# Kernel optimization log

Measured on AMD Instinct MI355X. Metric: run time of the kernel, lower is better.

The kernel has to match this reference:

```python
import jax, jax.numpy as jnp
import numpy as np

B, S, H, L = 32, 2048, 768, 9


def setup_inputs() -> dict:
    key = jax.random.key(0)
    k0, k1, k2, k3, k4, k5 = jax.random.split(key, 6)
    return {
        "hidden_states": jax.random.normal(k0, (B, S, H), jnp.float32),
        "W": jax.random.normal(k1, (L, H), jnp.float32) * 0.02,
        "b": jnp.zeros((L,), jnp.float32),
        "start_transitions": jax.random.uniform(k2, (L,), jnp.float32, -0.1, 0.1),
        "end_transitions": jax.random.uniform(k3, (L,), jnp.float32, -0.1, 0.1),
        "transitions": jax.random.uniform(k4, (L, L), jnp.float32, -0.1, 0.1),
        "labels": jax.random.randint(k5, (B, S), 0, L).astype(jnp.int64),
        "attention_mask": jnp.ones((B, S), jnp.int32),
    }


def _crf_neg_log_likelihood(emissions, tags, mask, start_transitions, end_transitions, transitions):
    # emissions: [B,S,L], tags: [B,S] int, mask: [B,S] bool (mask[:,0] assumed True)
    Bsz = emissions.shape[0]
    em_t = jnp.swapaxes(emissions, 0, 1)          # [S,B,L]
    tags_t = jnp.swapaxes(tags, 0, 1)             # [S,B]
    mask_t = jnp.swapaxes(mask, 0, 1).astype(emissions.dtype)  # [S,B]
    barange = jnp.arange(Bsz)

    # ---- numerator: score of the gold path (pytorch-crf _compute_score) ----
    score0 = start_transitions[tags_t[0]] + em_t[0][barange, tags_t[0]]  # [B]

    def num_step(score, x):
        em_i, tag_prev, tag_i, m_i = x
        step = transitions[tag_prev, tag_i] + em_i[barange, tag_i]
        return score + step * m_i, None

    score, _ = jax.lax.scan(num_step, score0,
                            (em_t[1:], tags_t[:-1], tags_t[1:], mask_t[1:]))
    seq_ends = jnp.sum(mask, axis=1).astype(jnp.int32) - 1              # [B]
    last_tags = jnp.take_along_axis(tags, seq_ends[:, None], axis=1)[:, 0]
    score = score + end_transitions[last_tags]

    # ---- denominator: log partition (forward algorithm) ----
    alpha0 = start_transitions[None, :] + em_t[0]  # [B,L]

    def den_step(alpha, x):
        em_i, m_i = x
        # alpha[b,i] + transitions[i,j] + em_i[b,j] -> logsumexp over i
        nxt = jax.nn.logsumexp(alpha[:, :, None] + transitions[None, :, :]
                               + em_i[:, None, :], axis=1)
        alpha = jnp.where(m_i[:, None] > 0, nxt, alpha)
        return alpha, None

    alpha, _ = jax.lax.scan(den_step, alpha0, (em_t[1:], mask_t[1:]))
    denom = jax.nn.logsumexp(alpha + end_transitions[None, :], axis=1)  # [B]

    llh = score - denom
    return -jnp.mean(llh)  # reduction='mean', loss = -log_likelihood


def reference(hidden_states, W, b, start_transitions, end_transitions, transitions, labels, attention_mask):
    # classifier over backbone hidden states
    emissions = jnp.einsum('bsh,lh->bsl', hidden_states, W) + b  # [B,S,L]
    label_mask = labels != -100
    lab = jnp.where(labels == -100, 0, labels)
    loss = _crf_neg_log_likelihood(emissions, lab, label_mask,
                                   start_transitions, end_transitions, transitions)
    return loss, emissions
```

## Files before the change

### kernel.cpp

```cpp
#include <hip/hip_runtime.h>

#define BB 32
#define SS 2048
#define HH 768
#define LL 9
#define NROWS (BB * SS)
#define NCHUNK 64
#define TCHUNK 32
#define PASSES 8
#define ROWS_PER_BLOCK 16
#define GEMM_BLOCKS (NROWS / ROWS_PER_BLOCK)

__device__ __forceinline__ float lse9(const float* v) {
  float m = fmaxf(fmaxf(fmaxf(fmaxf(v[0], v[1]), fmaxf(v[2], v[3])),
                        fmaxf(fmaxf(v[4], v[5]), fmaxf(v[6], v[7]))),
                  v[8]);
  float s = 0.f;
#pragma unroll
  for (int k = 0; k < 9; ++k) s += __expf(v[k] - m);
  return m + __logf(s);
}

template <int CTRL>
__device__ __forceinline__ float dpp_add(float x) {
  int t = __builtin_amdgcn_update_dpp(0, __float_as_int(x), CTRL, 0xf, 0xf, true);
  return x + __int_as_float(t);
}
__device__ __forceinline__ float red16(float x) {
  x = dpp_add<0xB1>(x);
  x = dpp_add<0x4E>(x);
  x = dpp_add<0x141>(x);
  x = dpp_add<0x140>(x);
  return x;
}

__global__ __launch_bounds__(256)
void emis_gemm(const float* __restrict__ hs, const float* __restrict__ W,
               const float* __restrict__ bias, float* __restrict__ em) {
  const int tid = threadIdx.x;
  const int lane = tid & 63;
  const int w = tid >> 6;
  const int pair = w >> 1;
  const int half = w & 1;
  const int rowbase = blockIdx.x * ROWS_PER_BLOCK;
  const int kb = half * 384;

  __shared__ float part[ROWS_PER_BLOCK][8][LL];

  float wr[LL][6];
#pragma unroll
  for (int l = 0; l < LL; ++l) {
    float4 t4 = *reinterpret_cast<const float4*>(W + l * HH + kb + lane * 4);
    float2 t2 = *reinterpret_cast<const float2*>(W + l * HH + kb + 256 + lane * 2);
    wr[l][0] = t4.x; wr[l][1] = t4.y; wr[l][2] = t4.z; wr[l][3] = t4.w;
    wr[l][4] = t2.x; wr[l][5] = t2.y;
  }

  const float* r0 = hs + (size_t)(rowbase + 0 * 2 + pair) * HH + kb;
  float4 a4 = *reinterpret_cast<const float4*>(r0 + lane * 4);
  float2 a2 = *reinterpret_cast<const float2*>(r0 + 256 + lane * 2);
  const float* r1 = hs + (size_t)(rowbase + 1 * 2 + pair) * HH + kb;
  float4 b4 = *reinterpret_cast<const float4*>(r1 + lane * 4);
  float2 b2 = *reinterpret_cast<const float2*>(r1 + 256 + lane * 2);

#pragma unroll
  for (int p = 0; p < PASSES; ++p) {
    float4 c4{};
    float2 c2{};
    if (p + 2 < PASSES) {
      const float* rn = hs + (size_t)(rowbase + (p + 2) * 2 + pair) * HH + kb;
      c4 = *reinterpret_cast<const float4*>(rn + lane * 4);
      c2 = *reinterpret_cast<const float2*>(rn + 256 + lane * 2);
    }
    const float h[6] = {a4.x, a4.y, a4.z, a4.w, a2.x, a2.y};
    if ((lane & 15) == 0) {
    }
    float acc[LL];
#pragma unroll
    for (int l = 0; l < LL; ++l) {
      float s = h[0] * wr[l][0];
#pragma unroll
      for (int q = 1; q < 6; ++q) s = fmaf(h[q], wr[l][q], s);
      acc[l] = red16(s);
    }
    if ((lane & 15) == 0) {
      const int pi = half * 4 + (lane >> 4);
      const int o = p * 2 + pair;
#pragma unroll
      for (int l = 0; l < LL; ++l) part[o][pi][l] = acc[l];
    }
    a4 = b4; a2 = b2; b4 = c4; b2 = c2;
  }
  __syncthreads();

  for (int j = tid; j < ROWS_PER_BLOCK * LL; j += 256) {
    const int o = j / LL, l = j - o * LL;
    float s = bias[l];
#pragma unroll
    for (int q = 0; q < 8; ++q) s += part[o][q][l];
    em[(size_t)(rowbase + o) * LL + l] = s;
  }
}

__global__ __launch_bounds__(128)
void crf_chunk(const float* __restrict__ em, const int* __restrict__ lab,
               const float* __restrict__ trans, const float* __restrict__ startT,
               float* __restrict__ Pout, float* __restrict__ numpart,
               int* __restrict__ cntpart) {
  const int blk = blockIdx.x;
  const int b = blk >> 6, c = blk & 63;
  const int tid = threadIdx.x;
  const int lane = tid & 63;
  const int wv = tid >> 6;
  __shared__ float em_s[TCHUNK * LL];
  __shared__ int lab_s[TCHUNK + 1];
  __shared__ float Pbuf[2][81];

  const int t0 = c * TCHUNK;
  const size_t ebase = (size_t)(b * SS + t0) * LL;
  for (int i = tid; i < TCHUNK * LL; i += 128) em_s[i] = em[ebase + i];
  if (tid <= TCHUNK) {
    int g = t0 - 1 + tid;
    lab_s[tid] = (g >= 0) ? lab[b * SS + g] : 0;
  }
  const int i9 = tid / 9, j9 = tid % 9;
  float tc[9];
  if (tid < 81) {
#pragma unroll
    for (int k = 0; k < 9; ++k) tc[k] = trans[k * 9 + j9];
  }
  __syncthreads();

  unsigned long long mb =
      __ballot((lane < 32) ? (lab_s[1 + lane] != -100) : false);
  unsigned mask32 = (unsigned)mb;

  if (wv == 1) {
    float sc = 0.f;
    if (lane < 32) {
      int lv = lab_s[1 + lane];
      int tg = (lv != -100) ? lv : 0;
      if (t0 + lane == 0) {
        sc = startT[tg] + em_s[tg];
      } else if (lv != -100) {
        int pv = lab_s[lane];
        int tp = (pv != -100) ? pv : 0;
        sc = trans[tp * LL + tg] + em_s[lane * LL + tg];
      }
    }
#pragma unroll
    for (int off = 32; off; off >>= 1) sc += __shfl_xor(sc, off, 64);
    if (lane == 0) {
      numpart[blk] = sc;
      cntpart[blk] = __popc(mask32);
    }
  }

  if (tid < 81) Pbuf[0][tid] = (i9 == j9) ? 0.f : -1e30f;
  __syncthreads();
  int cur = 0;
  const int ltstart = (c == 0) ? 1 : 0;
  for (int lt = ltstart; lt < TCHUNK; ++lt) {
    if ((mask32 >> lt) & 1u) {
      if (tid < 81) {
        float v[9];
#pragma unroll
        for (int k = 0; k < 9; ++k) v[k] = Pbuf[cur][i9 * 9 + k] + tc[k];
        Pbuf[cur ^ 1][tid] = lse9(v) + em_s[lt * LL + j9];
      }
      __syncthreads();
      cur ^= 1;
    }
  }
  if (tid < 81) Pout[(size_t)blk * 81 + tid] = Pbuf[cur][tid];
}

__global__ __launch_bounds__(128)
void crf_fold(const float* __restrict__ Pm, const float* __restrict__ em,
              const float* __restrict__ startT, const float* __restrict__ endT,
              const float* __restrict__ numpart, const int* __restrict__ cntpart,
              const int* __restrict__ lab, float* __restrict__ llh) {
  const int b = blockIdx.x, tid = threadIdx.x;
  __shared__ float Abuf[64 * 81];
  __shared__ float Bbuf[32 * 81];

  const float* src = Pm + (size_t)b * NCHUNK * 81;
  for (int i = tid; i < 64 * 81; i += 128) Abuf[i] = src[i];
  __syncthreads();

  float* pin = Abuf;
  float* pout = Bbuf;
  for (int n = 32;; n >>= 1) {
    for (int o = tid; o < n * 81; o += 128) {
      int m = o / 81, e = o % 81;
      int i = e / 9, j = e % 9;
      const float* M1 = pin + (2 * m) * 81;
      const float* M2 = pin + (2 * m + 1) * 81;
      float v[9];
#pragma unroll
      for (int k = 0; k < 9; ++k) v[k] = M1[i * 9 + k] + M2[k * 9 + j];
      pout[o] = lse9(v);
    }
    __syncthreads();
    if (n == 1) break;
    float* t = pin; pin = pout;
    pout = (pout == Bbuf) ? Abuf : t;
  }
  const float* fin = pout;

  float ns = 0.f;
  int cn = 0;
  if (tid < 64) {
    ns = numpart[b * 64 + tid];
    cn = cntpart[b * 64 + tid];
#pragma unroll
    for (int off = 32; off; off >>= 1) {
      ns += __shfl_xor(ns, off, 64);
      cn += __shfl_xor(cn, off, 64);
    }
  }
  if (tid == 0) {
    float a0[9], af[9], v[9];
#pragma unroll
    for (int j = 0; j < 9; ++j) a0[j] = startT[j] + em[(size_t)b * SS * LL + j];
#pragma unroll
    for (int j = 0; j < 9; ++j) {
#pragma unroll
      for (int k = 0; k < 9; ++k) v[k] = a0[k] + fin[k * 9 + j];
      af[j] = lse9(v);
    }
#pragma unroll
    for (int j = 0; j < 9; ++j) v[j] = af[j] + endT[j];
    float den = lse9(v);
    int se = cn - 1;
    int lt = lab[b * SS + se];
    if (lt == -100) lt = 0;
    llh[b] = (ns + endT[lt]) - den;
  }
}

__global__ __launch_bounds__(64)
void finalize(const float* __restrict__ llh, float* __restrict__ out) {
  int l = threadIdx.x;
  float v = (l < BB) ? llh[l] : 0.f;
#pragma unroll
  for (int off = 32; off; off >>= 1) v += __shfl_xor(v, off, 64);
  if (l == 0) out[0] = -v / (float)BB;
}

extern "C" void kernel_launch(void* const* d_in, const int* in_sizes, int n_in,
                              void* d_out, int out_size, void* d_ws, size_t ws_size,
                              hipStream_t stream) {
  const float* hs = (const float*)d_in[0];
  const float* W = (const float*)d_in[1];
  const float* bias = (const float*)d_in[2];
  const float* startT = (const float*)d_in[3];
  const float* endT = (const float*)d_in[4];
  const float* trans = (const float*)d_in[5];
  const int* labels = (const int*)d_in[6];

  float* out = (float*)d_out;
  float* em = out + 1;

  float* wsf = (float*)d_ws;
  float* numpart = wsf;
  int* cntpart = (int*)(wsf + 2048);
  float* Pm = wsf + 4096;
  float* llh = wsf + 4096 + 165888;

  emis_gemm<<<GEMM_BLOCKS, 256, 0, stream>>>(hs, W, bias, em);
  crf_chunk<<<BB * NCHUNK, 128, 0, stream>>>(em, labels, trans, startT,
                                             Pm, numpart, cntpart);
  crf_fold<<<BB, 128, 0, stream>>>(Pm, em, startT, endT, numpart, cntpart,
                                   labels, llh);
  finalize<<<1, 64, 0, stream>>>(llh, out);
}
```

Before: 77.88 us.

## Reduce GEMM partials via shared memory and fold finalize into crf_fold

The emission GEMM drops the DPP 16-lane reductions. Every lane now writes its partial dot products to a large shared array, and 72 threads then each sum 128 partials. Rows per block are halved and launch bounds request 4 blocks per CU, which raises the block count. The separate finalize kernel is removed by using an atomic counter in crf_fold, so the last block computes the mean; the Pm load is also vectorised to float4. The change trades cross-lane shuffles and a launch for much more LDS traffic and a long serial per-thread reduction.

New measurement: 82.51 us. 1.06x slower.

```diff
diff --git a/kernel.cpp b/kernel.cpp
--- a/kernel.cpp
+++ b/kernel.cpp
@@ -7,9 +7,9 @@
 #define NROWS (BB * SS)
 #define NCHUNK 64
 #define TCHUNK 32
-#define PASSES 8
-#define ROWS_PER_BLOCK 16
-#define GEMM_BLOCKS (NROWS / ROWS_PER_BLOCK)
+#define RPB 8
+#define PASSES 4
+#define GEMM_BLOCKS (NROWS / RPB)
 
 __device__ __forceinline__ float lse9(const float* v) {
   float m = fmaxf(fmaxf(fmaxf(fmaxf(v[0], v[1]), fmaxf(v[2], v[3])),
@@ -21,31 +21,20 @@
   return m + __logf(s);
 }
 
-template <int CTRL>
-__device__ __forceinline__ float dpp_add(float x) {
-  int t = __builtin_amdgcn_update_dpp(0, __float_as_int(x), CTRL, 0xf, 0xf, true);
-  return x + __int_as_float(t);
-}
-__device__ __forceinline__ float red16(float x) {
-  x = dpp_add<0xB1>(x);
-  x = dpp_add<0x4E>(x);
-  x = dpp_add<0x141>(x);
-  x = dpp_add<0x140>(x);
-  return x;
-}
-
-__global__ __launch_bounds__(256)
+__global__ __launch_bounds__(256, 4)
 void emis_gemm(const float* __restrict__ hs, const float* __restrict__ W,
-               const float* __restrict__ bias, float* __restrict__ em) {
+               const float* __restrict__ bias, float* __restrict__ em,
+               int* __restrict__ gcnt) {
   const int tid = threadIdx.x;
   const int lane = tid & 63;
   const int w = tid >> 6;
   const int pair = w >> 1;
   const int half = w & 1;
-  const int rowbase = blockIdx.x * ROWS_PER_BLOCK;
+  const int rowbase = blockIdx.x * RPB;
   const int kb = half * 384;
-
-  __shared__ float part[ROWS_PER_BLOCK][8][LL];
+  if (blockIdx.x == 0 && tid == 0) *gcnt = 0;
+
+  __shared__ float part[RPB][129][9];
 
   float wr[LL][6];
 #pragma unroll
@@ -56,48 +45,45 @@
     wr[l][4] = t2.x; wr[l][5] = t2.y;
   }
 
-  const float* r0 = hs + (size_t)(rowbase + 0 * 2 + pair) * HH + kb;
-  float4 a4 = *reinterpret_cast<const float4*>(r0 + lane * 4);
-  float2 a2 = *reinterpret_cast<const float2*>(r0 + 256 + lane * 2);
-  const float* r1 = hs + (size_t)(rowbase + 1 * 2 + pair) * HH + kb;
-  float4 b4 = *reinterpret_cast<const float4*>(r1 + lane * 4);
-  float2 b2 = *reinterpret_cast<const float2*>(r1 + 256 + lane * 2);
+  const int Lp = half * 64 + lane;
+  const float* rA = hs + (size_t)(rowbase + 0 + pair) * HH + kb;
+  float4 A4 = *reinterpret_cast<const float4*>(rA + lane * 4);
+  float2 A2 = *reinterpret_cast<const float2*>(rA + 256 + lane * 2);
+  const float* rB = hs + (size_t)(rowbase + 2 + pair) * HH + kb;
+  float4 B4 = *reinterpret_cast<const float4*>(rB + lane * 4);
+  float2 B2 = *reinterpret_cast<const float2*>(rB + 256 + lane * 2);
 
 #pragma unroll
   for (int p = 0; p < PASSES; ++p) {
-    float4 c4{};
-    float2 c2{};
+    float4 cur4 = (p & 1) ? B4 : A4;
+    float2 cur2 = (p & 1) ? B2 : A2;
     if (p + 2 < PASSES) {
       const float* rn = hs + (size_t)(rowbase + (p + 2) * 2 + pair) * HH + kb;
-      c4 = *reinterpret_cast<const float4*>(rn + lane * 4);
-      c2 = *reinterpret_cast<const float2*>(rn + 256 + lane * 2);
-    }
-    const float h[6] = {a4.x, a4.y, a4.z, a4.w, a2.x, a2.y};
-    if ((lane & 15) == 0) {
-    }
-    float acc[LL];
+      if (p & 1) {
+        B4 = *reinterpret_cast<const float4*>(rn + lane * 4);
+        B2 = *reinterpret_cast<const float2*>(rn + 256 + lane * 2);
+      } else {
+        A4 = *reinterpret_cast<const float4*>(rn + lane * 4);
+        A2 = *reinterpret_cast<const float2*>(rn + 256 + lane * 2);
+      }
+    }
+    const float h[6] = {cur4.x, cur4.y, cur4.z, cur4.w, cur2.x, cur2.y};
+    const int o = p * 2 + pair;
 #pragma unroll
     for (int l = 0; l < LL; ++l) {
       float s = h[0] * wr[l][0];
 #pragma unroll
       for (int q = 1; q < 6; ++q) s = fmaf(h[q], wr[l][q], s);
-      acc[l] = red16(s);
-    }
-    if ((lane & 15) == 0) {
-      const int pi = half * 4 + (lane >> 4);
-      const int o = p * 2 + pair;
-#pragma unroll
-      for (int l = 0; l < LL; ++l) part[o][pi][l] = acc[l];
-    }
-    a4 = b4; a2 = b2; b4 = c4; b2 = c2;
-  }
-  __syncthreads();
-
-  for (int j = tid; j < ROWS_PER_BLOCK * LL; j += 256) {
-    const int o = j / LL, l = j - o * LL;
+      part[o][Lp][l] = s;
+    }
+  }
+  __syncthreads();
+
+  if (tid < RPB * LL) {
+    const int o = tid / LL, l = tid - o * LL;
     float s = bias[l];
-#pragma unroll
-    for (int q = 0; q < 8; ++q) s += part[o][q][l];
+#pragma unroll 8
+    for (int q = 0; q < 128; ++q) s += part[o][q][l];
     em[(size_t)(rowbase + o) * LL + l] = s;
   }
 }
@@ -179,13 +165,15 @@
 void crf_fold(const float* __restrict__ Pm, const float* __restrict__ em,
               const float* __restrict__ startT, const float* __restrict__ endT,
               const float* __restrict__ numpart, const int* __restrict__ cntpart,
-              const int* __restrict__ lab, float* __restrict__ llh) {
+              const int* __restrict__ lab, float* __restrict__ llh,
+              int* __restrict__ gcnt, float* __restrict__ out) {
   const int b = blockIdx.x, tid = threadIdx.x;
-  __shared__ float Abuf[64 * 81];
-  __shared__ float Bbuf[32 * 81];
+  __shared__ __align__(16) float Abuf[64 * 81];
+  __shared__ __align__(16) float Bbuf[32 * 81];
 
   const float* src = Pm + (size_t)b * NCHUNK * 81;
-  for (int i = tid; i < 64 * 81; i += 128) Abuf[i] = src[i];
+  for (int i = tid; i < 64 * 81 / 4; i += 128)
+    reinterpret_cast<float4*>(Abuf)[i] = reinterpret_cast<const float4*>(src)[i];
   __syncthreads();
 
   float* pin = Abuf;
@@ -236,16 +224,18 @@
     int lt = lab[b * SS + se];
     if (lt == -100) lt = 0;
     llh[b] = (ns + endT[lt]) - den;
-  }
-}
-
-__global__ __launch_bounds__(64)
-void finalize(const float* __restrict__ llh, float* __restrict__ out) {
-  int l = threadIdx.x;
-  float v = (l < BB) ? llh[l] : 0.f;
-#pragma unroll
-  for (int off = 32; off; off >>= 1) v += __shfl_xor(v, off, 64);
-  if (l == 0) out[0] = -v / (float)BB;
+
+    __threadfence();
+    int old = atomicAdd(gcnt, 1);
+    if (old == BB - 1) {
+      __threadfence();
+      float s = 0.f;
+      for (int i = 0; i < BB; ++i)
+        s += __hip_atomic_load(&llh[i], __ATOMIC_RELAXED,
+                               __HIP_MEMORY_SCOPE_AGENT);
+      out[0] = -s / (float)BB;
+    }
+  }
 }
 
 extern "C" void kernel_launch(void* const* d_in, const int* in_sizes, int n_in,
@@ -263,15 +253,15 @@
   float* em = out + 1;
 
   float* wsf = (float*)d_ws;
-  float* numpart = wsf;
-  int* cntpart = (int*)(wsf + 2048);
-  float* Pm = wsf + 4096;
-  float* llh = wsf + 4096 + 165888;
-
-  emis_gemm<<<GEMM_BLOCKS, 256, 0, stream>>>(hs, W, bias, em);
+  float* llh = wsf;
+  int* gcnt = (int*)(wsf + 32);
+  float* numpart = wsf + 64;
+  int* cntpart = (int*)(wsf + 64 + 2048);
+  float* Pm = wsf + 64 + 4096;
+
+  emis_gemm<<<GEMM_BLOCKS, 256, 0, stream>>>(hs, W, bias, em, gcnt);
   crf_chunk<<<BB * NCHUNK, 128, 0, stream>>>(em, labels, trans, startT,
                                              Pm, numpart, cntpart);
   crf_fold<<<BB, 128, 0, stream>>>(Pm, em, startT, endT, numpart, cntpart,
-                                   labels, llh);
-  finalize<<<1, 64, 0, stream>>>(llh, out);
-}
+                                   labels, llh, gcnt, out);
+}
```
